# Performance work log

Measured on AMD Instinct MI355X. Metric: run time of the kernel, lower is better.

## Reference

```python
import jax, jax.numpy as jnp
import numpy as np

B, T = 1024, 64
FEAT, TENC, MAN, HID = 1024, 256, 128, 2048
IN_DIM = FEAT + TENC + MAN  # 1408


def setup_inputs() -> dict:
    key = jax.random.key(0)
    ks = jax.random.split(key, 9)
    s = 0.02
    return {
        "input_repr": jax.random.normal(ks[0], (B, T, FEAT), jnp.float32),
        "time_enc": jax.random.normal(ks[1], (B, TENC), jnp.float32),
        "y0": jax.random.normal(ks[2], (B, MAN), jnp.float32),
        "W_ih": jax.random.normal(ks[3], (4 * HID, IN_DIM), jnp.float32) * s,
        "b_ih": jax.random.normal(ks[4], (4 * HID,), jnp.float32) * s,
        "W_hh": jax.random.normal(ks[5], (4 * HID, HID), jnp.float32) * s,
        "b_hh": jax.random.normal(ks[6], (4 * HID,), jnp.float32) * s,
        "W_mu": jax.random.normal(ks[7], (MAN, HID), jnp.float32) * s,
        "b_mu": jax.random.normal(ks[8], (MAN,), jnp.float32) * s,
    }


def reference(input_repr, time_enc, y0, W_ih, b_ih, W_hh, b_hh, W_mu, b_mu):
    batch = input_repr.shape[0]
    hid = W_hh.shape[1]
    dtype = input_repr.dtype
    # steps t = 1..T-1, time-major for scan: (T-1, B, FEAT)
    xs = jnp.swapaxes(input_repr[:, 1:], 0, 1)
    h0 = jnp.zeros((batch, hid), dtype)
    c0 = jnp.zeros((batch, hid), dtype)

    def step(carry, x_t):
        h, c, y = carry
        rnn_in = jnp.concatenate([x_t, y, time_enc], axis=1)  # (B, IN_DIM)
        gates = rnn_in @ W_ih.T + b_ih + h @ W_hh.T + b_hh    # (B, 4H)
        i, f, g, o = jnp.split(gates, 4, axis=1)               # torch LSTMCell order
        c = jax.nn.sigmoid(f) * c + jax.nn.sigmoid(i) * jnp.tanh(g)
        h = jax.nn.sigmoid(o) * jnp.tanh(c)
        y = h @ W_mu.T + b_mu
        return (h, c, y), y

    _, ys = jax.lax.scan(step, (h0, c0, y0), xs)  # ys: (T-1, B, MAN)
    man = jnp.concatenate([y0[None], ys], axis=0)  # (T, B, MAN)
    return jnp.swapaxes(man, 0, 1)  # (B, T, MAN)
```

## Files before the change

### kernel.cpp

```cpp
#include <hip/hip_runtime.h>
#include <hip/hip_bf16.h>

#define B_ 1024
#define T_ 64
#define FEAT_ 1024
#define TENC_ 256
#define MAN_ 128
#define HID_ 2048
#define NG_ 8192
#define IND_ 1408

typedef __attribute__((ext_vector_type(8))) short short8;
typedef __attribute__((ext_vector_type(4))) float f32x4;

typedef const __attribute__((address_space(1))) void as1_cvoid;
typedef __attribute__((address_space(3))) void as3_void;

static __device__ __forceinline__ float sigmoidf_(float x) {
  return 1.0f / (1.0f + __expf(-x));
}
static __device__ __forceinline__ float tanh_fast(float x) {
  return 1.0f - 2.0f / (__expf(2.0f * x) + 1.0f);
}
static __device__ __forceinline__ unsigned short f2b(float x) {
  __hip_bfloat16 h = __float2bfloat16(x);
  return *reinterpret_cast<unsigned short*>(&h);
}
static __device__ __forceinline__ float b2f(unsigned short u) {
  unsigned int v = ((unsigned int)u) << 16;
  return *reinterpret_cast<float*>(&v);
}

static __device__ __forceinline__ int gate_perm(int p) {
  int h = ((p >> 7) << 5) + (((p >> 6) & 1) << 4) + (p & 15);
  int gate = (p >> 4) & 3;
  return gate * HID_ + h;
}

__device__ __forceinline__ void gload16(const unsigned short* g, unsigned short* l) {
  __builtin_amdgcn_global_load_lds((as1_cvoid*)g, (as3_void*)l, 16, 0, 0);
}


__global__ void zero_u32(unsigned int* p, long n) {
  long i = (long)blockIdx.x * blockDim.x + threadIdx.x;
  if (i < n) p[i] = 0u;
}

__global__ void pack_x_tm(const float* __restrict__ src, unsigned short* __restrict__ dst) {
  int c = threadIdx.x * 4;
  int bt = blockIdx.x;
  int b = bt >> 6, t = bt & 63;
  float4 v = *reinterpret_cast<const float4*>(&src[((long)b * T_ + t) * FEAT_ + c]);
  ushort4 o;
  o.x = f2b(v.x); o.y = f2b(v.y); o.z = f2b(v.z); o.w = f2b(v.w);
  *reinterpret_cast<ushort4*>(&dst[((long)t * B_ + b) * FEAT_ + c]) = o;
}

__global__ void pack_bf16(const float* __restrict__ src, long ld, long off,
                          unsigned short* __restrict__ dst, long cols) {
  long c = ((long)blockIdx.x * blockDim.x + threadIdx.x) * 4;
  if (c >= cols) return;
  long r = blockIdx.y;
  float4 v = *reinterpret_cast<const float4*>(&src[r * ld + off + c]);
  ushort4 o;
  o.x = f2b(v.x); o.y = f2b(v.y); o.z = f2b(v.z); o.w = f2b(v.w);
  *reinterpret_cast<ushort4*>(&dst[r * cols + c]) = o;
}

__global__ void pack_wih(const float* __restrict__ W_ih,
                         unsigned short* __restrict__ Wx,
                         unsigned short* __restrict__ Wy,
                         unsigned short* __restrict__ Wte) {
  int c = (blockIdx.x * 256 + threadIdx.x) * 4;
  if (c >= IND_) return;
  long rd = blockIdx.y;
  long rs = gate_perm((int)rd);
  float4 v = *reinterpret_cast<const float4*>(&W_ih[rs * IND_ + c]);
  ushort4 o;
  o.x = f2b(v.x); o.y = f2b(v.y); o.z = f2b(v.z); o.w = f2b(v.w);
  if (c < FEAT_) {
    *reinterpret_cast<ushort4*>(&Wx[rd * FEAT_ + c]) = o;
  } else if (c < FEAT_ + MAN_) {
    *reinterpret_cast<ushort4*>(&Wy[rd * MAN_ + (c - FEAT_)]) = o;
  } else {
    *reinterpret_cast<ushort4*>(&Wte[rd * TENC_ + (c - FEAT_ - MAN_)]) = o;
  }
}

__global__ void transpose_to_bf16(const float* __restrict__ src, unsigned short* __restrict__ dst) {
  int i = blockIdx.x * 256 + threadIdx.x;
  int n = i >> 7, m = i & 127;
  dst[i] = f2b(src[(long)m * HID_ + n]);
}

__global__ void bias_prep(const float* __restrict__ W_ih, const float* __restrict__ b_ih,
                          const float* __restrict__ b_hh, const float* __restrict__ b_mu,
                          float* __restrict__ bvec2, float* __restrict__ nbm) {
  int p = blockIdx.x * 256 + threadIdx.x;
  if (p >= NG_) return;
  int g = gate_perm(p);
  const float* wy = &W_ih[(long)g * IND_ + FEAT_];
  float s = 0.f;
  #pragma unroll 8
  for (int m = 0; m < MAN_; ++m) s += b_mu[m] * wy[m];
  bvec2[p] = b_ih[g] + b_hh[g] + s;
  nbm[p] = -s;
}

__global__ void out_t0(const float* __restrict__ y0, float* __restrict__ out) {
  int i = blockIdx.x * 256 + threadIdx.x;
  int b = i >> 7, m = i & 127;
  out[(long)b * (T_ * MAN_) + m] = y0[i];
}

template<int SMODE, int AMODE>
__global__ __launch_bounds__(256, 2)
void gemm_bt(const unsigned short* __restrict__ A1, long lda1,
             const unsigned short* __restrict__ A2, long lda2, int K1,
             const unsigned short* __restrict__ W1, const unsigned short* __restrict__ W2,
             int N, int K,
             const float* __restrict__ bias,
             const void* __restrict__ addmat, const void* __restrict__ addmat2,
             void* __restrict__ outp, long ldo,
             float* __restrict__ cstate, unsigned short* __restrict__ hout)
{
  __shared__ unsigned short As[128 * 64];
  __shared__ unsigned short Bs[128 * 64];
  const int tid = threadIdx.x, lane = tid & 63, wave = tid >> 6;
  const long bm = blockIdx.x, bn = blockIdx.y;

  f32x4 acc[4][4] = {};

  const int nkt = K >> 6;
  const int wm = wave >> 1, wn = wave & 1;
  const int lr = lane & 15, lq = lane >> 4;

  for (int kt = 0; kt < nkt; ++kt) {
    const int k0 = kt << 6;
    const unsigned short* Ab; long lda; const unsigned short* Wb; long ldw; int ko;
    if (k0 < K1) { Ab = A1; lda = lda1; Wb = W1; ldw = K1;      ko = k0; }
    else         { Ab = A2; lda = lda2; Wb = W2; ldw = K - K1;  ko = k0 - K1; }
    __syncthreads();
    #pragma unroll
    for (int it = 0; it < 4; ++it) {
      const int c0 = it * 256 + wave * 64;
      const int c = c0 + lane;
      const int row = c >> 3, sub = c & 7;
      gload16(Ab + (bm * 128 + row) * lda + ko + sub * 8, &As[c0 * 8]);
      gload16(Wb + (bn * 128 + row) * ldw + ko + sub * 8, &Bs[c0 * 8]);
    }
    __syncthreads();
    #pragma unroll
    for (int kk = 0; kk < 2; ++kk) {
      short8 av[4], bv[4];
      const int lk = kk * 32 + lq * 8;
      #pragma unroll
      for (int m = 0; m < 4; ++m)
        av[m] = *reinterpret_cast<const short8*>(&As[(wm * 64 + m * 16 + lr) * 64 + lk]);
      #pragma unroll
      for (int n = 0; n < 4; ++n)
        bv[n] = *reinterpret_cast<const short8*>(&Bs[(wn * 64 + n * 16 + lr) * 64 + lk]);
      #pragma unroll
      for (int m = 0; m < 4; ++m)
        #pragma unroll
        for (int n = 0; n < 4; ++n)
          acc[m][n] = __builtin_amdgcn_mfma_f32_16x16x32_bf16(av[m], bv[n], acc[m][n], 0, 0, 0);
    }
  }

  const long grp = bn * 128 + wn * 64;

  if constexpr (SMODE == 3) {
    const int hcol = (int)bn * 32 + wn * 16 + lr;
    #pragma unroll
    for (int m = 0; m < 4; ++m) {
      #pragma unroll
      for (int r2 = 0; r2 < 4; ++r2) {
        const long row = bm * 128 + wm * 64 + m * 16 + lq * 4 + r2;
        const long qbase = row * (long)N + grp + lr * 4;
        ushort4 tq = *reinterpret_cast<const ushort4*>(
            &((const unsigned short*)addmat2)[qbase]);
        float gi = acc[m][0][r2] + b2f(tq.x);
        float gf = acc[m][1][r2] + b2f(tq.y);
        float gg = acc[m][2][r2] + b2f(tq.z);
        float go = acc[m][3][r2] + b2f(tq.w);
        if (addmat) {
          ushort4 gq = *reinterpret_cast<const ushort4*>(
              &((const unsigned short*)addmat)[qbase]);
          gi += b2f(gq.x); gf += b2f(gq.y); gg += b2f(gq.z); go += b2f(gq.w);
        }
        const long ci = row * HID_ + hcol;
        float c = cstate[ci];
        c = sigmoidf_(gf) * c + sigmoidf_(gi) * tanh_fast(gg);
        cstate[ci] = c;
        hout[ci] = f2b(sigmoidf_(go) * tanh_fast(c));
      }
    }
    return;
  }

  if constexpr (SMODE == 4) {
    #pragma unroll
    for (int m = 0; m < 4; ++m) {
      #pragma unroll
      for (int r2 = 0; r2 < 4; ++r2) {
        const long row = bm * 128 + wm * 64 + m * 16 + lq * 4 + r2;
        float v[4];
        #pragma unroll
        for (int n = 0; n < 4; ++n) {
          const long col = grp + n * 16 + lr;
          v[n] = acc[m][n][r2] + (bias ? bias[col] : 0.0f);
        }
        if constexpr (AMODE == 5) {
          ushort4 a4 = *reinterpret_cast<const ushort4*>(
              &((const unsigned short*)addmat)[row * (long)N + grp + lr * 4]);
          v[0] += b2f(a4.x); v[1] += b2f(a4.y); v[2] += b2f(a4.z); v[3] += b2f(a4.w);
        }
        ushort4 o;
        o.x = f2b(v[0]); o.y = f2b(v[1]); o.z = f2b(v[2]); o.w = f2b(v[3]);
        *reinterpret_cast<ushort4*>(
            &reinterpret_cast<unsigned short*>(outp)[row * ldo + grp + lr * 4]) = o;
      }
    }
    return;
  }

  #pragma unroll
  for (int m = 0; m < 4; ++m) {
    #pragma unroll
    for (int n = 0; n < 4; ++n) {
      const long col = grp + n * 16 + lr;
      const float bvv = bias ? bias[col] : 0.0f;
      #pragma unroll
      for (int r2 = 0; r2 < 4; ++r2) {
        const long row = bm * 128 + wm * 64 + m * 16 + lq * 4 + r2;
        float v = acc[m][n][r2] + bvv;
        if constexpr (AMODE == 3) v += ((const float*)addmat)[(long)gate_perm((int)row) * N + col];
        if constexpr (SMODE == 0) {
          reinterpret_cast<float*>(outp)[row * ldo + col] = v;
        } else if constexpr (SMODE == 1) {
          reinterpret_cast<unsigned short*>(outp)[row * ldo + col] = f2b(v);
        } else {
          const long bb = row & 1023, tt = (row >> 10) + 1;
          reinterpret_cast<float*>(outp)[bb * (T_ * MAN_) + tt * MAN_ + col] = v;
        }
      }
    }
  }
}

__global__ __launch_bounds__(256, 2)
void step_fused(const unsigned short* __restrict__ Whh,
                const unsigned short* __restrict__ Wx,
                const unsigned short* __restrict__ Xt1,
                const unsigned short* __restrict__ xg_rd,
                unsigned short* __restrict__ xg_wr,
                const unsigned short* __restrict__ TBq,
                const unsigned short* __restrict__ hprev,
                unsigned short* __restrict__ hout,
                float* __restrict__ cstate)
{
  __shared__ unsigned short As[128 * 64];
  __shared__ unsigned short Bs[128 * 64];
  const int tid = threadIdx.x, lane = tid & 63, wave = tid >> 6;
  const int flat = (int)blockIdx.x;
  const bool isStep = flat < 512;
  const int f = isStep ? flat : flat - 512;
  const int j = f >> 3;
  const long bm = j >> 3;
  const long bn = (long)(f & 7) * 8 + (j & 7);
  const int wm = wave >> 1, wn = wave & 1;
  const int lr = lane & 15, lq = lane >> 4;

  const unsigned short* Abase = isStep ? hprev : Xt1;
  const unsigned short* Wbase = isStep ? Whh : Wx;
  const long lda = isStep ? HID_ : FEAT_;
  const int nkt = isStep ? (HID_ >> 6) : (FEAT_ >> 6);

  f32x4 acc[4][4] = {};

  for (int kt = 0; kt < nkt; ++kt) {
    const int ko = kt << 6;
    __syncthreads();
    #pragma unroll
    for (int it = 0; it < 4; ++it) {
      const int c0 = it * 256 + wave * 64;
      const int c = c0 + lane;
      const int row = c >> 3, sub = c & 7;
      gload16(Abase + (bm * 128 + row) * lda + ko + sub * 8, &As[c0 * 8]);
      gload16(Wbase + (bn * 128 + row) * lda + ko + sub * 8, &Bs[c0 * 8]);
    }
    __syncthreads();
    #pragma unroll
    for (int kk = 0; kk < 2; ++kk) {
      short8 av[4], bv[4];
      const int lk = kk * 32 + lq * 8;
      #pragma unroll
      for (int m = 0; m < 4; ++m)
        av[m] = *reinterpret_cast<const short8*>(&As[(wm * 64 + m * 16 + lr) * 64 + lk]);
      #pragma unroll
      for (int n = 0; n < 4; ++n)
        bv[n] = *reinterpret_cast<const short8*>(&Bs[(wn * 64 + n * 16 + lr) * 64 + lk]);
      #pragma unroll
      for (int m = 0; m < 4; ++m)
        #pragma unroll
        for (int n = 0; n < 4; ++n)
          acc[m][n] = __builtin_amdgcn_mfma_f32_16x16x32_bf16(av[m], bv[n], acc[m][n], 0, 0, 0);
    }
  }

  const long grp = bn * 128 + wn * 64;

  if (isStep) {
    const int hcol = (int)bn * 32 + wn * 16 + lr;
    #pragma unroll
    for (int m = 0; m < 4; ++m) {
      #pragma unroll
      for (int r2 = 0; r2 < 4; ++r2) {
        const long row = bm * 128 + wm * 64 + m * 16 + lq * 4 + r2;
        const long qbase = row * (long)NG_ + grp + lr * 4;
        ushort4 gq = *reinterpret_cast<const ushort4*>(&xg_rd[qbase]);
        ushort4 tq = *reinterpret_cast<const ushort4*>(&TBq[qbase]);
        float gi = acc[m][0][r2] + b2f(gq.x) + b2f(tq.x);
        float gf = acc[m][1][r2] + b2f(gq.y) + b2f(tq.y);
        float gg = acc[m][2][r2] + b2f(gq.z) + b2f(tq.z);
        float go = acc[m][3][r2] + b2f(gq.w) + b2f(tq.w);
        const long ci = row * HID_ + hcol;
        float c = cstate[ci];
        c = sigmoidf_(gf) * c + sigmoidf_(gi) * tanh_fast(gg);
        cstate[ci] = c;
        hout[ci] = f2b(sigmoidf_(go) * tanh_fast(c));
      }
    }
  } else {
    #pragma unroll
    for (int m = 0; m < 4; ++m) {
      #pragma unroll
      for (int r2 = 0; r2 < 4; ++r2) {
        const long row = bm * 128 + wm * 64 + m * 16 + lq * 4 + r2;
        ushort4 o;
        o.x = f2b(acc[m][0][r2]); o.y = f2b(acc[m][1][r2]);
        o.z = f2b(acc[m][2][r2]); o.w = f2b(acc[m][3][r2]);
        *reinterpret_cast<ushort4*>(&xg_wr[row * (long)NG_ + grp + lr * 4]) = o;
      }
    }
  }
}

extern "C" void kernel_launch(void* const* d_in, const int* in_sizes, int n_in,
                              void* d_out, int out_size, void* d_ws, size_t ws_size,
                              hipStream_t stream) {
  const float* input_repr = (const float*)d_in[0];
  const float* time_enc   = (const float*)d_in[1];
  const float* y0         = (const float*)d_in[2];
  const float* W_ih       = (const float*)d_in[3];
  const float* b_ih       = (const float*)d_in[4];
  const float* W_hh       = (const float*)d_in[5];
  const float* b_hh       = (const float*)d_in[6];
  const float* W_mu       = (const float*)d_in[7];
  const float* b_mu       = (const float*)d_in[8];
  float* out = (float*)d_out;

  char* ws = (char*)d_ws;
  auto alloc = [&](size_t bytes) {
    char* p = ws; ws += (bytes + 255) & ~(size_t)255; return p;
  };
  unsigned short* Xtm    = (unsigned short*)alloc((size_t)T_ * B_ * FEAT_ * 2);
  unsigned short* hstore = (unsigned short*)alloc((size_t)T_ * B_ * HID_ * 2);
  float*  cst   = (float*)alloc((size_t)B_ * HID_ * 4);
  unsigned short* TB2 = (unsigned short*)alloc((size_t)B_ * NG_ * 2);
  unsigned short* TB1 = (unsigned short*)alloc((size_t)B_ * NG_ * 2);
  unsigned short* Whhf  = (unsigned short*)alloc((size_t)NG_ * HID_ * 2);
  unsigned short* Wxbf  = (unsigned short*)alloc((size_t)NG_ * FEAT_ * 2);
  unsigned short* Wybf  = (unsigned short*)alloc((size_t)NG_ * MAN_ * 2);
  unsigned short* Wtebf = (unsigned short*)alloc((size_t)NG_ * TENC_ * 2);
  unsigned short* WmuT  = (unsigned short*)alloc((size_t)HID_ * MAN_ * 2);
  unsigned short* Wmubf = (unsigned short*)alloc((size_t)MAN_ * HID_ * 2);
  unsigned short* tebf  = (unsigned short*)alloc((size_t)B_ * TENC_ * 2);
  unsigned short* y0bf  = (unsigned short*)alloc((size_t)B_ * MAN_ * 2);
  float* bvec2 = (float*)alloc(NG_ * 4);
  float* nbm   = (float*)alloc(NG_ * 4);
  size_t base_bytes = (size_t)(ws - (char*)d_ws);
  size_t xg_bytes = (size_t)2 * B_ * NG_ * 2;
  bool use_xg = (base_bytes + xg_bytes + 4096) <= ws_size;
  unsigned short* xgring = use_xg ? (unsigned short*)alloc(xg_bytes) : nullptr;

  pack_x_tm<<<B_ * T_, 256, 0, stream>>>(input_repr, Xtm);
  pack_wih<<<dim3(2, NG_), 256, 0, stream>>>(W_ih, Wxbf, Wybf, Wtebf);
  pack_bf16<<<dim3(2, MAN_), 256, 0, stream>>>(W_mu, HID_, 0, Wmubf, HID_);
  pack_bf16<<<dim3(1, B_), 256, 0, stream>>>(time_enc, TENC_, 0, tebf, TENC_);
  pack_bf16<<<dim3(1, B_), 256, 0, stream>>>(y0, MAN_, 0, y0bf, MAN_);
  transpose_to_bf16<<<1024, 256, 0, stream>>>(W_mu, WmuT);
  bias_prep<<<NG_ / 256, 256, 0, stream>>>(W_ih, b_ih, b_hh, b_mu, bvec2, nbm);
  zero_u32<<<(B_ * HID_ / 2 + 255) / 256, 256, 0, stream>>>((unsigned int*)hstore, (long)B_ * HID_ / 2);
  zero_u32<<<(B_ * HID_ + 255) / 256, 256, 0, stream>>>((unsigned int*)cst, (long)B_ * HID_);
  out_t0<<<B_ * MAN_ / 256, 256, 0, stream>>>(y0, out);

  gemm_bt<1, 3><<<dim3(NG_ / 128, HID_ / 128), 256, 0, stream>>>(
      Wybf, MAN_, Wybf, MAN_, MAN_, WmuT, WmuT, HID_, MAN_,
      nullptr, W_hh, nullptr, Whhf, HID_, nullptr, nullptr);
  gemm_bt<4, 0><<<dim3(B_ / 128, NG_ / 128), 256, 0, stream>>>(
      tebf, TENC_, tebf, TENC_, TENC_, Wtebf, Wtebf, NG_, TENC_,
      bvec2, nullptr, nullptr, TB2, NG_, nullptr, nullptr);
  gemm_bt<4, 5><<<dim3(B_ / 128, NG_ / 128), 256, 0, stream>>>(
      y0bf, MAN_, y0bf, MAN_, MAN_, Wybf, Wybf, NG_, MAN_,
      nbm, TB2, nullptr, TB1, NG_, nullptr, nullptr);

  if (use_xg) {
    gemm_bt<4, 0><<<dim3(B_ / 128, NG_ / 128), 256, 0, stream>>>(
        Xtm + (long)B_ * FEAT_, FEAT_, Xtm, FEAT_, 1024,
        Wxbf, Wxbf, NG_, 1024,
        nullptr, nullptr, nullptr, xgring + (size_t)B_ * NG_, NG_, nullptr, nullptr);

    for (int t = 1; t < T_; ++t) {
      const bool hasxg = (t + 1 < T_);
      step_fused<<<hasxg ? 1024 : 512, 256, 0, stream>>>(
          Whhf, Wxbf,
          hasxg ? Xtm + (long)(t + 1) * B_ * FEAT_ : nullptr,
          xgring + (size_t)(t & 1) * B_ * NG_,
          hasxg ? xgring + (size_t)((t + 1) & 1) * B_ * NG_ : nullptr,
          (t == 1 ? TB1 : TB2),
          hstore + (long)(t - 1) * B_ * HID_,
          hstore + (long)t * B_ * HID_,
          cst);
    }
  } else {
    for (int t = 1; t < T_; ++t) {
      const unsigned short* A1 = Xtm + (long)t * B_ * FEAT_;
      const unsigned short* A2 = hstore + (long)(t - 1) * B_ * HID_;
      gemm_bt<3, 0><<<dim3(B_ / 128, NG_ / 128), 256, 0, stream>>>(
          A1, FEAT_, A2, HID_, FEAT_,
          Wxbf, Whhf, NG_, FEAT_ + HID_,
          nullptr, nullptr, (t == 1 ? TB1 : TB2), nullptr, 0,
          cst, hstore + (long)t * B_ * HID_);
    }
  }

  gemm_bt<2, 0><<<dim3((T_ - 1) * B_ / 128, MAN_ / 128), 256, 0, stream>>>(
      hstore + (long)B_ * HID_, HID_, hstore + (long)B_ * HID_, HID_, HID_,
      Wmubf, Wmubf, MAN_, HID_,
      b_mu, nullptr, nullptr, out, 0, nullptr, nullptr);
}
```

Before: 4.367 ms.

## Quantize recurrent W_hh and hidden state to FP8 for step GEMM

Quantizes the combined recurrent weight to per-row scaled FP8 and keeps an FP8 copy of the hidden state in a ring buffer, so the recurrent step GEMM uses FP8 MFMA with 128-wide K tiles. The goal is to halve the memory traffic of the recurrent GEMM and double its MFMA throughput. Scales are applied in the epilogue. The trade-off is lower numerical precision, which over 63 recurrent steps could drift past tolerance, plus an extra FP8 write of h on every step.

```diff
diff --git a/kernel.cpp b/kernel.cpp
--- a/kernel.cpp
+++ b/kernel.cpp
@@ -31,13 +31,28 @@
   return *reinterpret_cast<float*>(&v);
 }
 
+static __device__ __forceinline__ unsigned char f2fp8(float x) {
+  unsigned int u = __float_as_uint(x);
+  unsigned char s = (unsigned char)((u >> 31) << 7);
+  float a = fabsf(x);
+  if (a >= 448.f) return s | 0x7E;
+  if (a < 0.015625f) {
+    int q = (int)rintf(a * 512.f);
+    return s | (unsigned char)q;
+  }
+  unsigned int b = __float_as_uint(a) + 0x80000;
+  int e = (int)(b >> 23) - 127;
+  unsigned int m = (b >> 20) & 7;
+  return s | (unsigned char)(((e + 7) << 3) | m);
+}
+
 static __device__ __forceinline__ int gate_perm(int p) {
   int h = ((p >> 7) << 5) + (((p >> 6) & 1) << 4) + (p & 15);
   int gate = (p >> 4) & 3;
   return gate * HID_ + h;
 }
 
-__device__ __forceinline__ void gload16(const unsigned short* g, unsigned short* l) {
+__device__ __forceinline__ void gload16(const void* g, void* l) {
   __builtin_amdgcn_global_load_lds((as1_cvoid*)g, (as3_void*)l, 16, 0, 0);
 }
 
@@ -112,6 +127,37 @@
   int i = blockIdx.x * 256 + threadIdx.x;
   int b = i >> 7, m = i & 127;
   out[(long)b * (T_ * MAN_) + m] = y0[i];
+}
+
+__global__ void quant_w8(const unsigned short* __restrict__ Wbf,
+                         unsigned char* __restrict__ W8,
+                         float* __restrict__ invs) {
+  const int row = blockIdx.x;
+  const unsigned short* wr = Wbf + (long)row * HID_;
+  const int i0 = threadIdx.x * 8;
+  short8 v = *reinterpret_cast<const short8*>(&wr[i0]);
+  float mx = 0.f;
+  #pragma unroll
+  for (int j = 0; j < 8; ++j) mx = fmaxf(mx, fabsf(b2f((unsigned short)v[j])));
+  #pragma unroll
+  for (int o = 32; o > 0; o >>= 1) mx = fmaxf(mx, __shfl_down(mx, o));
+  __shared__ float red[4];
+  if ((threadIdx.x & 63) == 0) red[threadIdx.x >> 6] = mx;
+  __syncthreads();
+  float m4 = fmaxf(fmaxf(red[0], red[1]), fmaxf(red[2], red[3]));
+  float scale, inv;
+  if (m4 < 1e-30f) { scale = 0.f; inv = 0.f; }
+  else {
+    int e = ilogbf(m4);
+    scale = ldexpf(1.f, 7 - e);
+    inv = ldexpf(1.f, e - 15);
+  }
+  if (threadIdx.x == 0) invs[row] = inv;
+  unsigned long long packed = 0;
+  #pragma unroll
+  for (int j = 0; j < 8; ++j)
+    packed |= (unsigned long long)f2fp8(b2f((unsigned short)v[j]) * scale) << (8 * j);
+  *reinterpret_cast<unsigned long long*>(&W8[(long)row * HID_ + i0]) = packed;
 }
 
 template<int SMODE, int AMODE>
@@ -251,18 +297,19 @@
 }
 
 __global__ __launch_bounds__(256, 2)
-void step_fused(const unsigned short* __restrict__ Whh,
+void step_fused(const unsigned char* __restrict__ Whh8,
+                const float* __restrict__ invs,
                 const unsigned short* __restrict__ Wx,
                 const unsigned short* __restrict__ Xt1,
                 const unsigned short* __restrict__ xg_rd,
                 unsigned short* __restrict__ xg_wr,
                 const unsigned short* __restrict__ TBq,
-                const unsigned short* __restrict__ hprev,
+                const unsigned char* __restrict__ h8_rd,
+                unsigned char* __restrict__ h8_wr,
                 unsigned short* __restrict__ hout,
                 float* __restrict__ cstate)
 {
-  __shared__ unsigned short As[128 * 64];
-  __shared__ unsigned short Bs[128 * 64];
+  __shared__ unsigned char smem[32768];
   const int tid = threadIdx.x, lane = tid & 63, wave = tid >> 6;
   const int flat = (int)blockIdx.x;
   const bool isStep = flat < 512;
@@ -272,48 +319,45 @@
   const long bn = (long)(f & 7) * 8 + (j & 7);
   const int wm = wave >> 1, wn = wave & 1;
   const int lr = lane & 15, lq = lane >> 4;
-
-  const unsigned short* Abase = isStep ? hprev : Xt1;
-  const unsigned short* Wbase = isStep ? Whh : Wx;
-  const long lda = isStep ? HID_ : FEAT_;
-  const int nkt = isStep ? (HID_ >> 6) : (FEAT_ >> 6);
+  const long grp = bn * 128 + wn * 64;
 
   f32x4 acc[4][4] = {};
 
-  for (int kt = 0; kt < nkt; ++kt) {
-    const int ko = kt << 6;
-    __syncthreads();
-    #pragma unroll
-    for (int it = 0; it < 4; ++it) {
-      const int c0 = it * 256 + wave * 64;
-      const int c = c0 + lane;
-      const int row = c >> 3, sub = c & 7;
-      gload16(Abase + (bm * 128 + row) * lda + ko + sub * 8, &As[c0 * 8]);
-      gload16(Wbase + (bn * 128 + row) * lda + ko + sub * 8, &Bs[c0 * 8]);
-    }
-    __syncthreads();
-    #pragma unroll
-    for (int kk = 0; kk < 2; ++kk) {
-      short8 av[4], bv[4];
-      const int lk = kk * 32 + lq * 8;
-      #pragma unroll
-      for (int m = 0; m < 4; ++m)
-        av[m] = *reinterpret_cast<const short8*>(&As[(wm * 64 + m * 16 + lr) * 64 + lk]);
-      #pragma unroll
-      for (int n = 0; n < 4; ++n)
-        bv[n] = *reinterpret_cast<const short8*>(&Bs[(wn * 64 + n * 16 + lr) * 64 + lk]);
-      #pragma unroll
-      for (int m = 0; m < 4; ++m)
+  if (isStep) {
+    unsigned char* As = smem;
+    unsigned char* Bs = smem + 16384;
+    for (int kt = 0; kt < HID_ / 128; ++kt) {
+      const int ko = kt << 7;
+      __syncthreads();
+      #pragma unroll
+      for (int it = 0; it < 4; ++it) {
+        const int c0 = it * 256 + wave * 64;
+        const int c = c0 + lane;
+        const int row = c >> 3, sub = c & 7;
+        gload16(h8_rd + (bm * 128 + row) * HID_ + ko + sub * 16, As + c0 * 16);
+        gload16(Whh8  + (bn * 128 + row) * HID_ + ko + sub * 16, Bs + c0 * 16);
+      }
+      __syncthreads();
+      #pragma unroll
+      for (int kk = 0; kk < 4; ++kk) {
+        long av[4], bv[4];
+        const int lk = kk * 32 + lq * 8;
+        #pragma unroll
+        for (int m = 0; m < 4; ++m)
+          av[m] = *reinterpret_cast<const long*>(As + (wm * 64 + m * 16 + lr) * 128 + lk);
         #pragma unroll
         for (int n = 0; n < 4; ++n)
-          acc[m][n] = __builtin_amdgcn_mfma_f32_16x16x32_bf16(av[m], bv[n], acc[m][n], 0, 0, 0);
-    }
-  }
-
-  const long grp = bn * 128 + wn * 64;
-
-  if (isStep) {
+          bv[n] = *reinterpret_cast<const long*>(Bs + (wn * 64 + n * 16 + lr) * 128 + lk);
+        #pragma unroll
+        for (int m = 0; m < 4; ++m)
+          #pragma unroll
+          for (int n = 0; n < 4; ++n)
+            acc[m][n] = __builtin_amdgcn_mfma_f32_16x16x32_fp8_fp8(av[m], bv[n], acc[m][n], 0, 0, 0);
+      }
+    }
+
     const int hcol = (int)bn * 32 + wn * 16 + lr;
+    const float4 invq = *reinterpret_cast<const float4*>(&invs[grp + lr * 4]);
     #pragma unroll
     for (int m = 0; m < 4; ++m) {
       #pragma unroll
@@ -322,18 +366,51 @@
         const long qbase = row * (long)NG_ + grp + lr * 4;
         ushort4 gq = *reinterpret_cast<const ushort4*>(&xg_rd[qbase]);
         ushort4 tq = *reinterpret_cast<const ushort4*>(&TBq[qbase]);
-        float gi = acc[m][0][r2] + b2f(gq.x) + b2f(tq.x);
-        float gf = acc[m][1][r2] + b2f(gq.y) + b2f(tq.y);
-        float gg = acc[m][2][r2] + b2f(gq.z) + b2f(tq.z);
-        float go = acc[m][3][r2] + b2f(gq.w) + b2f(tq.w);
+        float gi = acc[m][0][r2] * invq.x + b2f(gq.x) + b2f(tq.x);
+        float gf = acc[m][1][r2] * invq.y + b2f(gq.y) + b2f(tq.y);
+        float gg = acc[m][2][r2] * invq.z + b2f(gq.z) + b2f(tq.z);
+        float go = acc[m][3][r2] * invq.w + b2f(gq.w) + b2f(tq.w);
         const long ci = row * HID_ + hcol;
         float c = cstate[ci];
         c = sigmoidf_(gf) * c + sigmoidf_(gi) * tanh_fast(gg);
         cstate[ci] = c;
-        hout[ci] = f2b(sigmoidf_(go) * tanh_fast(c));
+        float h = sigmoidf_(go) * tanh_fast(c);
+        hout[ci] = f2b(h);
+        h8_wr[ci] = f2fp8(h * 256.f);
       }
     }
   } else {
+    unsigned short* As = (unsigned short*)smem;
+    unsigned short* Bs = (unsigned short*)(smem + 16384);
+    for (int kt = 0; kt < FEAT_ / 64; ++kt) {
+      const int ko = kt << 6;
+      __syncthreads();
+      #pragma unroll
+      for (int it = 0; it < 4; ++it) {
+        const int c0 = it * 256 + wave * 64;
+        const int c = c0 + lane;
+        const int row = c >> 3, sub = c & 7;
+        gload16(Xt1 + (bm * 128 + row) * FEAT_ + ko + sub * 8, &As[c0 * 8]);
+        gload16(Wx  + (bn * 128 + row) * FEAT_ + ko + sub * 8, &Bs[c0 * 8]);
+      }
+      __syncthreads();
+      #pragma unroll
+      for (int kk = 0; kk < 2; ++kk) {
+        short8 av[4], bv[4];
+        const int lk = kk * 32 + lq * 8;
+        #pragma unroll
+        for (int m = 0; m < 4; ++m)
+          av[m] = *reinterpret_cast<const short8*>(&As[(wm * 64 + m * 16 + lr) * 64 + lk]);
+        #pragma unroll
+        for (int n = 0; n < 4; ++n)
+          bv[n] = *reinterpret_cast<const short8*>(&Bs[(wn * 64 + n * 16 + lr) * 64 + lk]);
+        #pragma unroll
+        for (int m = 0; m < 4; ++m)
+          #pragma unroll
+          for (int n = 0; n < 4; ++n)
+            acc[m][n] = __builtin_amdgcn_mfma_f32_16x16x32_bf16(av[m], bv[n], acc[m][n], 0, 0, 0);
+      }
+    }
     #pragma unroll
     for (int m = 0; m < 4; ++m) {
       #pragma unroll
@@ -381,6 +458,9 @@
   unsigned short* y0bf  = (unsigned short*)alloc((size_t)B_ * MAN_ * 2);
   float* bvec2 = (float*)alloc(NG_ * 4);
   float* nbm   = (float*)alloc(NG_ * 4);
+  unsigned char* Whh8 = (unsigned char*)alloc((size_t)NG_ * HID_);
+  float* invs = (float*)alloc(NG_ * 4);
+  unsigned char* h8ring = (unsigned char*)alloc((size_t)2 * B_ * HID_);
   size_t base_bytes = (size_t)(ws - (char*)d_ws);
   size_t xg_bytes = (size_t)2 * B_ * NG_ * 2;
   bool use_xg = (base_bytes + xg_bytes + 4096) <= ws_size;
@@ -394,12 +474,14 @@
   transpose_to_bf16<<<1024, 256, 0, stream>>>(W_mu, WmuT);
   bias_prep<<<NG_ / 256, 256, 0, stream>>>(W_ih, b_ih, b_hh, b_mu, bvec2, nbm);
   zero_u32<<<(B_ * HID_ / 2 + 255) / 256, 256, 0, stream>>>((unsigned int*)hstore, (long)B_ * HID_ / 2);
+  zero_u32<<<(B_ * HID_ / 4 + 255) / 256, 256, 0, stream>>>((unsigned int*)h8ring, (long)B_ * HID_ / 4);
   zero_u32<<<(B_ * HID_ + 255) / 256, 256, 0, stream>>>((unsigned int*)cst, (long)B_ * HID_);
   out_t0<<<B_ * MAN_ / 256, 256, 0, stream>>>(y0, out);
 
   gemm_bt<1, 3><<<dim3(NG_ / 128, HID_ / 128), 256, 0, stream>>>(
       Wybf, MAN_, Wybf, MAN_, MAN_, WmuT, WmuT, HID_, MAN_,
       nullptr, W_hh, nullptr, Whhf, HID_, nullptr, nullptr);
+  quant_w8<<<NG_, 256, 0, stream>>>(Whhf, Whh8, invs);
   gemm_bt<4, 0><<<dim3(B_ / 128, NG_ / 128), 256, 0, stream>>>(
       tebf, TENC_, tebf, TENC_, TENC_, Wtebf, Wtebf, NG_, TENC_,
       bvec2, nullptr, nullptr, TB2, NG_, nullptr, nullptr);
@@ -416,12 +498,13 @@
     for (int t = 1; t < T_; ++t) {
       const bool hasxg = (t + 1 < T_);
       step_fused<<<hasxg ? 1024 : 512, 256, 0, stream>>>(
-          Whhf, Wxbf,
+          Whh8, invs, Wxbf,
           hasxg ? Xtm + (long)(t + 1) * B_ * FEAT_ : nullptr,
           xgring + (size_t)(t & 1) * B_ * NG_,
           hasxg ? xgring + (size_t)((t + 1) & 1) * B_ * NG_ : nullptr,
           (t == 1 ? TB1 : TB2),
-          hstore + (long)(t - 1) * B_ * HID_,
+          h8ring + (size_t)((t - 1) & 1) * B_ * HID_,
+          h8ring + (size_t)(t & 1) * B_ * HID_,
           hstore + (long)t * B_ * HID_,
           cst);
     }
```

After: 9.430 ms. 2.16x slower.
